# Optimization experiments

Hardware: AMD Instinct MI355X
Metric: run time of the kernel (lower is better)

Reference implementation:

```python
import jax, jax.numpy as jnp
import numpy as np

SCALE = 0.0625      # spatial_scale
OUT = 7             # out_size (== part_size)
C_OUT = 256         # output_dim (== input channels, group_size=1)
SPP = 4             # sample_per_part
TRANS_STD = 0.1
FC_DIM = 1024
B, H, W = 4, 128, 128
N_ROI = 2000
IMG = 2048.0        # H / SCALE


def _round_half(x):
    # CUDA round(): half away from zero (coords are non-negative here)
    return jnp.floor(x + 0.5)


def deform_roi_pool(data, rois, offset):
    """Faithful port of deform_roi_pooling (DCNv2 deform PS-ROI pooling, group_size=1).
    data: [B,C,H,W]; rois: [N,5]; offset: None or [N,2,OUT,OUT]. Returns [N,C,OUT,OUT]."""
    Bn, C, Hh, Ww = data.shape
    N = rois.shape[0]
    b = rois[:, 0].astype(jnp.int32)
    sw = _round_half(rois[:, 1]) * SCALE - 0.5
    sh = _round_half(rois[:, 2]) * SCALE - 0.5
    ew = (_round_half(rois[:, 3]) + 1.0) * SCALE - 0.5
    eh = (_round_half(rois[:, 4]) + 1.0) * SCALE - 0.5
    rw = jnp.maximum(ew - sw, 0.1)
    rh = jnp.maximum(eh - sh, 0.1)
    bw, bh = rw / OUT, rh / OUT              # bin sizes
    subw, subh = bw / SPP, bh / SPP          # sub-bin sizes

    ph, pw = jnp.meshgrid(jnp.arange(OUT, dtype=data.dtype),
                          jnp.arange(OUT, dtype=data.dtype), indexing='ij')
    wstart = pw[None] * bw[:, None, None] + sw[:, None, None]   # [N,OUT,OUT]
    hstart = ph[None] * bh[:, None, None] + sh[:, None, None]
    if offset is not None:
        # part_size == out_size -> part index == bin index
        wstart = wstart + offset[:, 0] * TRANS_STD * rw[:, None, None]
        hstart = hstart + offset[:, 1] * TRANS_STD * rh[:, None, None]

    ih2, iw2 = jnp.meshgrid(jnp.arange(SPP, dtype=data.dtype),
                            jnp.arange(SPP, dtype=data.dtype), indexing='ij')
    ih2, iw2 = ih2.reshape(-1), iw2.reshape(-1)  # [SPP*SPP]
    # sample coords [S2, N, OUT, OUT]
    ws = wstart[None] + iw2[:, None, None, None] * subw[None, :, None, None]
    hs = hstart[None] + ih2[:, None, None, None] * subh[None, :, None, None]

    bb = b[:, None, None]  # [N,1,1]

    def body(carry, coords):
        acc, cnt = carry
        w, h = coords                                 # [N,OUT,OUT]
        valid = (w >= -0.5) & (w <= Ww - 0.5) & (h >= -0.5) & (h <= Hh - 0.5)
        wc = jnp.clip(w, 0.0, Ww - 1.0)
        hc = jnp.clip(h, 0.0, Hh - 1.0)
        x0 = jnp.floor(wc).astype(jnp.int32)
        y0 = jnp.floor(hc).astype(jnp.int32)
        x1 = jnp.minimum(x0 + 1, Ww - 1)
        y1 = jnp.minimum(y0 + 1, Hh - 1)
        dx = wc - x0
        dy = hc - y0
        v00 = data[bb, :, y0, x0]   # [N,OUT,OUT,C]
        v01 = data[bb, :, y0, x1]
        v10 = data[bb, :, y1, x0]
        v11 = data[bb, :, y1, x1]
        val = (((1 - dx) * (1 - dy))[..., None] * v00
               + (dx * (1 - dy))[..., None] * v01
               + ((1 - dx) * dy)[..., None] * v10
               + (dx * dy)[..., None] * v11)
        val = jnp.where(valid[..., None], val, 0.0)
        return (acc + val, cnt + valid.astype(data.dtype)), None

    init = (jnp.zeros((N, OUT, OUT, C), data.dtype),
            jnp.zeros((N, OUT, OUT), data.dtype))
    (s, cnt), _ = jax.lax.scan(body, init, (ws, hs))
    out = jnp.where(cnt[..., None] > 0, s / jnp.maximum(cnt, 1.0)[..., None], 0.0)
    return jnp.transpose(out, (0, 3, 1, 2))  # [N,C,OUT,OUT]


def setup_inputs() -> dict:
    key = jax.random.key(0)
    ks = jax.random.split(key, 16)
    data = jax.random.normal(ks[0], (B, C_OUT, H, W), dtype=jnp.float32)
    bidx = jax.random.randint(ks[1], (N_ROI,), 0, B).astype(jnp.float32)
    x1 = jax.random.uniform(ks[2], (N_ROI,), minval=0.0, maxval=IMG - 64.0)
    y1 = jax.random.uniform(ks[3], (N_ROI,), minval=0.0, maxval=IMG - 64.0)
    wbox = jax.random.uniform(ks[4], (N_ROI,), minval=16.0, maxval=400.0)
    hbox = jax.random.uniform(ks[5], (N_ROI,), minval=16.0, maxval=400.0)
    rois = jnp.stack([bidx, x1, y1,
                      jnp.minimum(x1 + wbox, IMG - 1.0),
                      jnp.minimum(y1 + hbox, IMG - 1.0)], axis=1)
    fin = OUT * OUT * C_OUT  # 12544
    def lin(k, i, o, s=None):
        s = (1.0 / np.sqrt(i)) if s is None else s
        return jax.random.normal(k, (i, o), dtype=jnp.float32) * s
    return {
        'data': data, 'rois': rois,
        'w1': lin(ks[6], fin, FC_DIM), 'b1': jnp.zeros((FC_DIM,), jnp.float32),
        'w2': lin(ks[7], FC_DIM, FC_DIM), 'b2': jnp.zeros((FC_DIM,), jnp.float32),
        'w3': lin(ks[8], FC_DIM, OUT * OUT * 2, 0.01), 'b3': jnp.zeros((OUT * OUT * 2,), jnp.float32),
        'mw1': lin(ks[9], fin, FC_DIM), 'mb1': jnp.zeros((FC_DIM,), jnp.float32),
        'mw2': lin(ks[10], FC_DIM, OUT * OUT, 0.01), 'mb2': jnp.zeros((OUT * OUT,), jnp.float32),
    }


def reference(data, rois, w1, b1, w2, b2, w3, b3, mw1, mb1, mw2, mb2):
    n = rois.shape[0]
    x = deform_roi_pool(data, rois, None)              # [N,C,OUT,OUT]
    xf = x.reshape(n, -1)
    h = jax.nn.relu(xf @ w1 + b1)
    h = jax.nn.relu(h @ w2 + b2)
    offset = (h @ w3 + b3).reshape(n, 2, OUT, OUT)
    m = jax.nn.relu(xf @ mw1 + mb1)
    mask = jax.nn.sigmoid(m @ mw2 + mb2).reshape(n, 1, OUT, OUT)
    feat = deform_roi_pool(data, rois, offset) * mask
    return feat
```

## Files before the change

kernel.cpp:

```cpp
#include <hip/hip_runtime.h>
#include <math.h>

#define WDIM 128
#define HDIM 128
#define BDIM 4
#define CDIM 256
#define NROI 2000
#define MPAD 2048
#define FIN  12544
#define FC   1024
#define HWC  (HDIM * WDIM * CDIM)

typedef unsigned short bf16r;
typedef unsigned short u16;
typedef __attribute__((ext_vector_type(8))) short bf16x8;
typedef __attribute__((ext_vector_type(4))) float f32x4;
typedef __attribute__((ext_vector_type(8))) _Float16 half8;
typedef __attribute__((ext_vector_type(8))) unsigned short ushort8v;

__device__ __forceinline__ bf16r f2bf(float f) {
    unsigned u = __float_as_uint(f);
    u += 0x7FFFu + ((u >> 16) & 1u);
    return (bf16r)(u >> 16);
}
__device__ __forceinline__ u16 f2h(float f) {
    union { u16 s; _Float16 h; } c; c.h = (_Float16)f; return c.s;
}

__device__ __forceinline__ void async16(const bf16r* g, bf16r* l) {
    __builtin_amdgcn_global_load_lds(
        (const __attribute__((address_space(1))) unsigned int*)g,
        (__attribute__((address_space(3))) unsigned int*)l, 16, 0, 0);
}

__device__ __forceinline__ void roi_geom(const float* __restrict__ rois, int n,
                                         int& b, float& sw, float& sh,
                                         float& rw, float& rh) {
    const float* r = rois + (size_t)n * 5;
    b = (int)r[0];
    float r1 = floorf(r[1] + 0.5f);
    float r2 = floorf(r[2] + 0.5f);
    float r3 = floorf(r[3] + 0.5f);
    float r4 = floorf(r[4] + 0.5f);
    sw = r1 * 0.0625f - 0.5f;
    sh = r2 * 0.0625f - 0.5f;
    float ew = (r3 + 1.0f) * 0.0625f - 0.5f;
    float eh = (r4 + 1.0f) * 0.0625f - 0.5f;
    rw = fmaxf(ew - sw, 0.1f);
    rh = fmaxf(eh - sh, 0.1f);
}

__device__ __forceinline__ void build_geometry(
        int n, int tid, const float* __restrict__ rois,
        const float* __restrict__ offs,
        const float* __restrict__ maskb,
        float* axW, unsigned* axMeta, uint2* wpix, int* npx, float* scale) {
    if (tid < 98) {
        int po = tid >> 1, axis = tid & 1;
        int b; float sw, sh, rw, rh;
        roi_geom(rois, n, b, sw, sh, rw, rh);
        float bw = rw * (1.f / 7.f), bh = rh * (1.f / 7.f);
        int ph = po / 7, pw = po - ph * 7;
        float start, sub;
        if (axis == 0) {
            start = (float)pw * bw + sw;
            if (offs) start += offs[(size_t)n * 98 + po] * 0.1f * rw;
            sub = bw * 0.25f;
        } else {
            start = (float)ph * bh + sh;
            if (offs) start += offs[(size_t)n * 98 + 49 + po] * 0.1f * rh;
            sub = bh * 0.25f;
        }
        float wsl[5] = {0.f, 0.f, 0.f, 0.f, 0.f};
        int base = 0, cnt = 0, mx = 0, any = 0;
#pragma unroll
        for (int i = 0; i < 4; ++i) {
            float p = start + (float)i * sub;
            bool valid = (p >= -0.5f) & (p <= 127.5f);
            float pc = fminf(fmaxf(p, 0.f), 127.f);
            int p0 = (int)floorf(pc);
            float d = pc - (float)p0;
            int p1 = min(p0 + 1, 127);
            if (valid) {
                if (!any) { base = p0; any = 1; }
                int c0 = p0 - base, c1 = p1 - base;
                float w0 = 1.f - d;
#pragma unroll
                for (int k = 0; k < 5; ++k)
                    wsl[k] += ((c0 == k) ? w0 : 0.f) + ((c1 == k) ? d : 0.f);
                cnt++;
                mx = max(mx, c1);
            }
        }
        int N = any ? mx + 1 : 0;
        axMeta[tid] = (unsigned)(N | (cnt << 3) | (base << 6));
#pragma unroll
        for (int k = 0; k < 5; ++k) axW[tid * 5 + k] = wsl[k];
    }
    __syncthreads();
    if (tid < 245) {
        int po = tid / 5, r = tid - po * 5;
        unsigned mx_ = axMeta[po * 2], my_ = axMeta[po * 2 + 1];
        int NX = mx_ & 7, NY = my_ & 7;
        int bx = (mx_ >> 6) & 127, by = (my_ >> 6) & 127;
        if (r == 0) {
            int cntx = (mx_ >> 3) & 7, cnty = (my_ >> 3) & 7;
            int ct = cntx * cnty;
            float sc = (ct > 0) ? 1.f / (float)ct : 0.f;
            if (maskb) sc *= (ct > 0) ? maskb[(size_t)n * 49 + po] : 0.f;
            npx[po] = NX * NY;
            scale[po] = sc;
        }
        if (r < NY) {
            float wyr = axW[(po * 2 + 1) * 5 + r];
            unsigned rowoff = (unsigned)(((by + r) * 128 + bx) * 512);
#pragma unroll
            for (int c = 0; c < 5; ++c)
                if (c < NX)
                    wpix[po * 28 + r * NX + c] =
                        make_uint2(rowoff + (unsigned)c * 512u,
                                   __float_as_uint(wyr * axW[po * 2 * 5 + c]));
        }
    }
    __syncthreads();
}

__global__ __launch_bounds__(256) void transpose_kernel(const float* __restrict__ data,
                                                        u16* __restrict__ data_t) {
    __shared__ float t[32][33];
    int x0 = blockIdx.x << 5;
    int c0 = blockIdx.y << 5;
    int b  = blockIdx.z >> 7;
    int y  = blockIdx.z & 127;
    int tx = threadIdx.x, ty = threadIdx.y;
#pragma unroll
    for (int i = 0; i < 32; i += 8)
        t[ty + i][tx] = data[(((size_t)b * CDIM + c0 + ty + i) * HDIM + y) * WDIM + x0 + tx];
    __syncthreads();
#pragma unroll
    for (int i = 0; i < 32; i += 8)
        data_t[(((size_t)b * HDIM + y) * WDIM + x0 + ty + i) * CDIM + c0 + tx] = f2h(t[tx][ty + i]);
}

__global__ __launch_bounds__(256) void conv_kernel(const float* __restrict__ srcA,
                                                   const float* __restrict__ srcB,
                                                   int nsplit, int ncols, int Nout,
                                                   int K, int perm,
                                                   bf16r* __restrict__ dst) {
    __shared__ float t[32][33];
    int k0 = blockIdx.x << 5, n0 = blockIdx.y << 5;
    int tx = threadIdx.x & 31, ty = threadIdx.x >> 5;
#pragma unroll
    for (int i = 0; i < 32; i += 8) {
        int k = k0 + ty + i;
        int n = n0 + tx;
        const float* s = (n < nsplit) ? srcA : srcB;
        int col = (n < nsplit) ? n : n - nsplit;
        int row = perm ? ((k & 255) * 49 + (k >> 8)) : k;
        float v = (n < Nout && col < ncols) ? s[(size_t)row * ncols + col] : 0.f;
        t[ty + i][tx] = v;
    }
    __syncthreads();
#pragma unroll
    for (int i = 0; i < 32; i += 8) {
        int n = n0 + ty + i;
        if (n < Nout) dst[(size_t)n * K + k0 + tx] = f2bf(t[tx][ty + i]);
    }
}

__global__ __launch_bounds__(512) void pool1_kernel(const u16* __restrict__ data_t,
                                                    const float* __restrict__ rois,
                                                    bf16r* __restrict__ xf) {
    __shared__ float axW[98 * 5];
    __shared__ unsigned axMeta[98];
    __shared__ uint2 wpix[49 * 28];
    __shared__ int npx[49];
    __shared__ float scale[49];
    int n = blockIdx.x, tid = threadIdx.x;
    build_geometry(n, tid, rois, nullptr, nullptr, axW, axMeta, wpix, npx, scale);
    int b = (int)rois[(size_t)n * 5];
    int wave = tid >> 6, lane = tid & 63, shalf = lane >> 5, c8 = (lane & 31) << 3;
    const char* dpb = (const char*)(data_t + (size_t)b * HWC + c8);
    for (int po = wave * 2 + shalf; po < 49; po += 16) {
        int npe = npx[po];
        float sc = scale[po];
        const uint2* wp = wpix + po * 28;
        float a[8];
#pragma unroll
        for (int k = 0; k < 8; ++k) a[k] = 0.f;
        int p = 0;
        for (; p + 2 <= npe; p += 2) {
            uint2 q0 = wp[p], q1 = wp[p + 1];
            half8 v0 = *(const half8*)(dpb + q0.x);
            half8 v1 = *(const half8*)(dpb + q1.x);
            float w0 = __uint_as_float(q0.y), w1 = __uint_as_float(q1.y);
#pragma unroll
            for (int k = 0; k < 8; ++k) a[k] += w0 * (float)v0[k];
#pragma unroll
            for (int k = 0; k < 8; ++k) a[k] += w1 * (float)v1[k];
        }
        if (p < npe) {
            uint2 q0 = wp[p];
            half8 v0 = *(const half8*)(dpb + q0.x);
            float w0 = __uint_as_float(q0.y);
#pragma unroll
            for (int k = 0; k < 8; ++k) a[k] += w0 * (float)v0[k];
        }
        ushort8v o;
#pragma unroll
        for (int k = 0; k < 8; ++k) o[k] = f2bf(a[k] * sc);
        *(ushort8v*)(xf + (size_t)n * FIN + po * 256 + c8) = o;
    }
}

__global__ __launch_bounds__(512) void pool2_kernel(const u16* __restrict__ data_t,
                                                    const float* __restrict__ rois,
                                                    const float* __restrict__ offs,
                                                    const float* __restrict__ maskb,
                                                    float* __restrict__ out) {
    __shared__ float tile[49 * 128];
    __shared__ float axW[98 * 5];
    __shared__ unsigned axMeta[98];
    __shared__ uint2 wpix[49 * 28];
    __shared__ int npx[49];
    __shared__ float scale[49];
    int n = blockIdx.x, chalf = blockIdx.y, tid = threadIdx.x;
    build_geometry(n, tid, rois, offs, maskb, axW, axMeta, wpix, npx, scale);
    int b = (int)rois[(size_t)n * 5];
    int wave = tid >> 6, lane = tid & 63, q = lane >> 4, c8 = (lane & 15) << 3;
    const char* dpb = (const char*)(data_t + (size_t)b * HWC + chalf * 128 + c8);
    for (int po = wave * 4 + q; po < 49; po += 32) {
        int npe = npx[po];
        float sc = scale[po];
        const uint2* wp = wpix + po * 28;
        float a[8];
#pragma unroll
        for (int k = 0; k < 8; ++k) a[k] = 0.f;
        int p = 0;
        for (; p + 2 <= npe; p += 2) {
            uint2 q0 = wp[p], q1 = wp[p + 1];
            half8 v0 = *(const half8*)(dpb + q0.x);
            half8 v1 = *(const half8*)(dpb + q1.x);
            float w0 = __uint_as_float(q0.y), w1 = __uint_as_float(q1.y);
#pragma unroll
            for (int k = 0; k < 8; ++k) a[k] += w0 * (float)v0[k];
#pragma unroll
            for (int k = 0; k < 8; ++k) a[k] += w1 * (float)v1[k];
        }
        if (p < npe) {
            uint2 q0 = wp[p];
            half8 v0 = *(const half8*)(dpb + q0.x);
            float w0 = __uint_as_float(q0.y);
#pragma unroll
            for (int k = 0; k < 8; ++k) a[k] += w0 * (float)v0[k];
        }
        int cs = c8 ^ ((po & 7) << 3);
        float4 lo = make_float4(a[0] * sc, a[1] * sc, a[2] * sc, a[3] * sc);
        float4 hi = make_float4(a[4] * sc, a[5] * sc, a[6] * sc, a[7] * sc);
        *(float4*)&tile[po * 128 + cs] = lo;
        *(float4*)&tile[po * 128 + cs + 4] = hi;
    }
    __syncthreads();
    float* op = out + (size_t)n * FIN + (size_t)chalf * 6272;
    for (int i = tid; i < 6272; i += 512) {
        int c = i / 49, po = i - c * 49;
        op[i] = tile[po * 128 + (c ^ ((po & 7) << 3))];
    }
}

__global__ __launch_bounds__(256) void gemm_mfma_kernel(
        const bf16r* __restrict__ A, int lda,
        const bf16r* __restrict__ Bt, int K,
        float* __restrict__ P, int Npad, int KS) {
    __shared__ bf16r As[128 * 32];
    __shared__ bf16r Bs[128 * 32];
    int tid = threadIdx.x;
    int wave = tid >> 6, lane = tid & 63;
    int m0 = blockIdx.y << 7, n0 = blockIdx.x << 7;
    int z = blockIdx.z;

    int srow = lane >> 2;
    int kchunk = ((lane & 3) ^ ((lane >> 3) & 3)) << 3;
    const bf16r* aG0 = A + (size_t)(m0 + wave * 32 + srow) * lda + kchunk;
    const bf16r* aG1 = A + (size_t)(m0 + wave * 32 + 16 + srow) * lda + kchunk;
    const bf16r* bG0 = Bt + (size_t)(n0 + wave * 32 + srow) * K + kchunk;
    const bf16r* bG1 = Bt + (size_t)(n0 + wave * 32 + 16 + srow) * K + kchunk;
    bf16r* aL0 = As + wave * 1024;
    bf16r* aL1 = As + wave * 1024 + 512;
    bf16r* bL0 = Bs + wave * 1024;
    bf16r* bL1 = Bs + wave * 1024 + 512;

    int l15 = lane & 15, quad = lane >> 4;
    int wr = wave >> 1, wc = wave & 1;
    int psw = (quad ^ ((l15 >> 1) & 3)) << 3;
    int aoff[4], boff[4];
#pragma unroll
    for (int t = 0; t < 4; ++t) {
        aoff[t] = ((wr * 64 + t * 16 + l15) * 32 + psw) * 2;
        boff[t] = ((wc * 64 + t * 16 + l15) * 32 + psw) * 2;
    }

    f32x4 acc[4][4];
#pragma unroll
    for (int i = 0; i < 4; ++i)
#pragma unroll
        for (int j = 0; j < 4; ++j) acc[i][j] = (f32x4){0.f, 0.f, 0.f, 0.f};

    int iters = K >> 5;
    int i0 = (int)((long)iters * z / KS);
    int i1 = (int)((long)iters * (z + 1) / KS);

    {
        size_t k0 = (size_t)i0 << 5;
        async16(aG0 + k0, aL0); async16(aG1 + k0, aL1);
        async16(bG0 + k0, bL0); async16(bG1 + k0, bL1);
    }
    for (int it = i0; it < i1; ++it) {
        __syncthreads();
        bf16x8 af[4], bfv[4];
#pragma unroll
        for (int t = 0; t < 4; ++t) af[t] = *(const bf16x8*)((const char*)As + aoff[t]);
#pragma unroll
        for (int t = 0; t < 4; ++t) bfv[t] = *(const bf16x8*)((const char*)Bs + boff[t]);
        __syncthreads();
        if (it + 1 < i1) {
            size_t k0 = (size_t)(it + 1) << 5;
            async16(aG0 + k0, aL0); async16(aG1 + k0, aL1);
            async16(bG0 + k0, bL0); async16(bG1 + k0, bL1);
        }
#pragma unroll
        for (int i = 0; i < 4; ++i)
#pragma unroll
            for (int j = 0; j < 4; ++j)
                acc[i][j] = __builtin_amdgcn_mfma_f32_16x16x32_bf16(af[i], bfv[j], acc[i][j], 0, 0, 0);
    }

    float* Pp = P + (size_t)z * MPAD * Npad;
#pragma unroll
    for (int i = 0; i < 4; ++i) {
        int row = m0 + wr * 64 + i * 16 + quad * 4;
#pragma unroll
        for (int j = 0; j < 4; ++j) {
            int col = n0 + wc * 64 + j * 16 + l15;
            float* o = Pp + (size_t)row * Npad + col;
#pragma unroll
            for (int r = 0; r < 4; ++r) o[(size_t)r * Npad] = acc[i][j][r];
        }
    }
}

__global__ __launch_bounds__(256) void reduce_kernel(
        const float* __restrict__ P, int shift, int KS,
        const float* __restrict__ bias0, const float* __restrict__ bias1, int bsplit,
        void* __restrict__ Out, int ldo, int M, int Nreal, int outmode) {
    int idx = blockIdx.x * 256 + threadIdx.x;
    int Npad = 1 << shift;
    int row = idx >> shift, col = idx & (Npad - 1);
    float s = 0.f;
    size_t plane = (size_t)MPAD << shift;
    for (int zz = 0; zz < KS; ++zz) s += P[(size_t)zz * plane + idx];
    if (row < M && col < Nreal) {
        float b = (col < bsplit) ? bias0[col] : bias1[col - bsplit];
        float v = s + b;
        if (outmode == 0) {
            v = fmaxf(v, 0.f);
            ((bf16r*)Out)[(size_t)row * ldo + col] = f2bf(v);
        } else {
            if (outmode == 2) v = 1.f / (1.f + expf(-v));
            ((float*)Out)[(size_t)row * ldo + col] = v;
        }
    }
}

extern "C" void kernel_launch(void* const* d_in, const int* in_sizes, int n_in,
                              void* d_out, int out_size, void* d_ws, size_t ws_size,
                              hipStream_t stream) {
    const float* data = (const float*)d_in[0];
    const float* rois = (const float*)d_in[1];
    const float* w1   = (const float*)d_in[2];
    const float* b1   = (const float*)d_in[3];
    const float* w2   = (const float*)d_in[4];
    const float* b2   = (const float*)d_in[5];
    const float* w3   = (const float*)d_in[6];
    const float* b3   = (const float*)d_in[7];
    const float* mw1  = (const float*)d_in[8];
    const float* mb1  = (const float*)d_in[9];
    const float* mw2  = (const float*)d_in[10];
    const float* mb2  = (const float*)d_in[11];
    float* out = (float*)d_out;

    char* w = (char*)d_ws;
    size_t off = 0;
    auto carve = [&](size_t bytes) {
        void* p = w + off;
        off += (bytes + 255) & ~(size_t)255;
        return p;
    };
    u16* data_t   = (u16*)carve((size_t)BDIM * HDIM * WDIM * CDIM * 2);
    bf16r* xf     = (bf16r*)carve((size_t)MPAD * FIN * 2);
    bf16r* bt1    = (bf16r*)carve((size_t)MPAD * FIN * 2);
    bf16r* hm     = (bf16r*)carve((size_t)MPAD * 2048 * 2);
    bf16r* h2     = (bf16r*)carve((size_t)MPAD * 1024 * 2);
    bf16r* bt2    = (bf16r*)carve((size_t)1024 * 1024 * 2);
    bf16r* bt3    = (bf16r*)carve((size_t)128 * 1024 * 2);
    bf16r* bt4    = (bf16r*)carve((size_t)128 * 1024 * 2);
    float* offs   = (float*)carve((size_t)NROI * 98 * 4);
    float* maskb  = (float*)carve((size_t)NROI * 49 * 4);
    float* P      = (float*)carve((size_t)3 * MPAD * 2048 * 4);

    conv_kernel<<<dim3(392, 64), 256, 0, stream>>>(w1, mw1, 1024, 1024, 2048, FIN, 1, bt1);
    conv_kernel<<<dim3(32, 32), 256, 0, stream>>>(w2, w2, 1 << 30, 1024, 1024, 1024, 0, bt2);
    conv_kernel<<<dim3(32, 4), 256, 0, stream>>>(w3, w3, 1 << 30, 98, 98, 1024, 0, bt3);
    conv_kernel<<<dim3(32, 2), 256, 0, stream>>>(mw2, mw2, 1 << 30, 49, 49, 1024, 0, bt4);
    transpose_kernel<<<dim3(4, 8, 512), dim3(32, 8), 0, stream>>>(data, data_t);
    pool1_kernel<<<dim3(NROI), 512, 0, stream>>>(data_t, rois, xf);

    gemm_mfma_kernel<<<dim3(16, 16, 3), 256, 0, stream>>>(xf, FIN, bt1, FIN, P, 2048, 3);
    reduce_kernel<<<16384, 256, 0, stream>>>(P, 11, 3, b1, mb1, 1024, hm, 2048, NROI, 2048, 0);
    gemm_mfma_kernel<<<dim3(8, 16, 4), 256, 0, stream>>>(hm, 2048, bt2, 1024, P, 1024, 4);
    reduce_kernel<<<8192, 256, 0, stream>>>(P, 10, 4, b2, b2, 1 << 30, h2, 1024, NROI, 1024, 0);
    gemm_mfma_kernel<<<dim3(1, 16, 8), 256, 0, stream>>>(h2, 1024, bt3, 1024, P, 128, 8);
    reduce_kernel<<<1024, 256, 0, stream>>>(P, 7, 8, b3, b3, 1 << 30, offs, 98, NROI, 98, 1);
    gemm_mfma_kernel<<<dim3(1, 16, 8), 256, 0, stream>>>(hm + 1024, 2048, bt4, 1024, P, 128, 8);
    reduce_kernel<<<1024, 256, 0, stream>>>(P, 7, 8, mb2, mb2, 1 << 30, maskb, 49, NROI, 49, 2);

    pool2_kernel<<<dim3(NROI, 2), 512, 0, stream>>>(data_t, rois, offs, maskb, out);
}
```

Measured before the change: 571.3 us.

## Add 256x256-tile 8-wave MFMA GEMM with ping-pong LDS staging for first FC layer

```diff
diff --git a/kernel.cpp b/kernel.cpp
--- a/kernel.cpp
+++ b/kernel.cpp
@@ -32,6 +32,9 @@
         (const __attribute__((address_space(1))) unsigned int*)g,
         (__attribute__((address_space(3))) unsigned int*)l, 16, 0, 0);
 }
+
+#define VMW(n) asm volatile("s_waitcnt vmcnt(" #n ")" ::: "memory")
+#define BARRIER() __builtin_amdgcn_s_barrier()
 
 __device__ __forceinline__ void roi_geom(const float* __restrict__ rois, int n,
                                          int& b, float& sw, float& sh,
@@ -268,6 +271,119 @@
     }
 }
 
+#define STAGE_A(buf, h, kt) do { \
+    async16(Abase + (size_t)(kt) * 64 + sAoff[h][0], &lds[buf][0][((h) * 128 + wave * 8) * 64]); \
+    async16(Abase + (size_t)(kt) * 64 + sAoff[h][1], &lds[buf][0][((h) * 128 + 64 + wave * 8) * 64]); \
+} while (0)
+#define STAGE_B(buf, h, kt) do { \
+    async16(Bbase + (size_t)(kt) * 64 + sBoff[h][0], &lds[buf][1][((h) * 128 + wave * 8) * 64]); \
+    async16(Bbase + (size_t)(kt) * 64 + sBoff[h][1], &lds[buf][1][((h) * 128 + 64 + wave * 8) * 64]); \
+} while (0)
+#define PHASE(buf, mh, nh, STAGE_STMT, GUARD_STMT) do { \
+    const char* Ar = (const char*)&lds[buf][0][0] + aQ + (mh) * 16384; \
+    const char* Br = (const char*)&lds[buf][1][0] + bQ + (nh) * 16384; \
+    bf16x8 af[4][2], bfv[2][2]; \
+    _Pragma("unroll") for (int i = 0; i < 4; ++i) \
+        _Pragma("unroll") for (int ks = 0; ks < 2; ++ks) \
+            af[i][ks] = *(const bf16x8*)(Ar + i * 2048 + fRB[ks]); \
+    _Pragma("unroll") for (int jf = 0; jf < 2; ++jf) \
+        _Pragma("unroll") for (int ks = 0; ks < 2; ++ks) \
+            bfv[jf][ks] = *(const bf16x8*)(Br + jf * 2048 + fRB[ks]); \
+    STAGE_STMT; \
+    BARRIER(); \
+    __builtin_amdgcn_s_setprio(1); \
+    _Pragma("unroll") for (int i = 0; i < 4; ++i) \
+        _Pragma("unroll") for (int jf = 0; jf < 2; ++jf) \
+            _Pragma("unroll") for (int ks = 0; ks < 2; ++ks) \
+                acc[(mh) * 4 + i][(nh) * 2 + jf] = __builtin_amdgcn_mfma_f32_16x16x32_bf16( \
+                    af[i][ks], bfv[jf][ks], acc[(mh) * 4 + i][(nh) * 2 + jf], 0, 0, 0); \
+    __builtin_amdgcn_s_setprio(0); \
+    GUARD_STMT; \
+    BARRIER(); \
+} while (0)
+
+__global__ __launch_bounds__(512, 2) void gemm256_kernel(
+        const bf16r* __restrict__ A, int lda,
+        const bf16r* __restrict__ Bt, int ldb,
+        float* __restrict__ P, int Npad, int KS, int ktiles) {
+    __shared__ bf16r lds[2][2][256 * 64];
+    int tid = threadIdx.x;
+    int wave = tid >> 6, lane = tid & 63;
+    int l15 = lane & 15, quad = lane >> 4;
+    int wm = wave >> 2, wn = wave & 3;
+
+    int idx = blockIdx.x + gridDim.x * blockIdx.y;
+    int nid = (idx & 7) * ((gridDim.x * gridDim.y) >> 3) + (idx >> 3);
+    int bx = nid % gridDim.x, by = nid / gridDim.x;
+    int m0 = by << 8, n0 = bx << 8;
+    int z = blockIdx.z;
+
+    int sAoff[2][2], sBoff[2][2];
+#pragma unroll
+    for (int h = 0; h < 2; ++h)
+#pragma unroll
+        for (int j = 0; j < 2; ++j) {
+            int slot = h * 128 + j * 64 + wave * 8 + (lane >> 3);
+            int g = (lane & 7) ^ ((slot >> 1) & 7);
+            int rowA = ((slot >> 6) & 1) * 128 + (slot >> 7) * 64 + (slot & 63);
+            int colB = ((slot >> 5) & 3) * 64 + (slot >> 7) * 32 + (slot & 31);
+            sAoff[h][j] = rowA * lda + g * 8;
+            sBoff[h][j] = colB * ldb + g * 8;
+        }
+    const bf16r* Abase = A + (size_t)m0 * lda;
+    const bf16r* Bbase = Bt + (size_t)n0 * ldb;
+
+    int fRB[2];
+#pragma unroll
+    for (int ks = 0; ks < 2; ++ks)
+        fRB[ks] = l15 * 128 + ((((ks << 2) + quad) ^ ((l15 >> 1) & 7)) << 4);
+    int aQ = wm * 8192;
+    int bQ = wn * 4096;
+
+    f32x4 acc[8][4];
+#pragma unroll
+    for (int i = 0; i < 8; ++i)
+#pragma unroll
+        for (int j = 0; j < 4; ++j) acc[i][j] = (f32x4){0.f, 0.f, 0.f, 0.f};
+
+    int tb = ((ktiles * z) / KS) & ~1;
+    int te = (z == KS - 1) ? ktiles : ((ktiles * (z + 1)) / KS) & ~1;
+    int nit = (te - tb) >> 1;
+
+    STAGE_A(0, 0, tb); STAGE_B(0, 0, tb); STAGE_A(0, 1, tb); STAGE_B(0, 1, tb);
+    STAGE_A(1, 0, tb + 1); STAGE_B(1, 0, tb + 1);
+    VMW(4);
+    BARRIER();
+
+    for (int it = 0; it < nit; ++it) {
+        int t1 = tb + 2 * it + 1, nx0 = t1 + 1, nx1 = t1 + 2;
+        bool last = (it == nit - 1);
+        PHASE(0, 0, 0, { STAGE_A(1, 1, t1); }, {});
+        PHASE(0, 0, 1, { STAGE_B(1, 1, t1); }, {});
+        PHASE(0, 1, 0, { if (!last) STAGE_A(0, 0, nx0); }, {});
+        PHASE(0, 1, 1, { if (!last) STAGE_B(0, 0, nx0); },
+              { if (last) { VMW(0); } else { VMW(4); } });
+        PHASE(1, 0, 0, { if (!last) STAGE_A(0, 1, nx0); }, {});
+        PHASE(1, 0, 1, { if (!last) STAGE_B(0, 1, nx0); }, {});
+        PHASE(1, 1, 0, { if (!last) STAGE_A(1, 0, nx1); }, {});
+        PHASE(1, 1, 1, { if (!last) STAGE_B(1, 0, nx1); },
+              { if (!last) { VMW(4); } });
+    }
+
+    float* Pp = P + (size_t)z * MPAD * Npad;
+#pragma unroll
+    for (int I = 0; I < 8; ++I) {
+        int row = m0 + wm * 128 + I * 16 + quad * 4;
+#pragma unroll
+        for (int J = 0; J < 4; ++J) {
+            int col = n0 + wn * 64 + J * 16 + l15;
+            float* o = Pp + (size_t)row * Npad + col;
+#pragma unroll
+            for (int r = 0; r < 4; ++r) o[(size_t)r * Npad] = acc[I][J][r];
+        }
+    }
+}
+
 __global__ __launch_bounds__(256) void gemm_mfma_kernel(
         const bf16r* __restrict__ A, int lda,
         const bf16r* __restrict__ Bt, int K,
@@ -276,7 +392,12 @@
     __shared__ bf16r Bs[128 * 32];
     int tid = threadIdx.x;
     int wave = tid >> 6, lane = tid & 63;
-    int m0 = blockIdx.y << 7, n0 = blockIdx.x << 7;
+    int nwgxy = gridDim.x * gridDim.y;
+    int idx = blockIdx.x + gridDim.x * blockIdx.y;
+    int chunk = nwgxy >> 3;
+    int nid = (idx & 7) * chunk + (idx >> 3);
+    int bx = nid % gridDim.x, by = nid / gridDim.x;
+    int m0 = by << 7, n0 = bx << 7;
     int z = blockIdx.z;
 
     int srow = lane >> 2;
@@ -406,7 +527,10 @@
     bf16r* bt4    = (bf16r*)carve((size_t)128 * 1024 * 2);
     float* offs   = (float*)carve((size_t)NROI * 98 * 4);
     float* maskb  = (float*)carve((size_t)NROI * 49 * 4);
-    float* P      = (float*)carve((size_t)3 * MPAD * 2048 * 4);
+    float* P      = (float*)(w + off);
+    size_t plane  = (size_t)MPAD * 2048 * 4;
+    size_t avail  = (ws_size > off) ? ws_size - off : 0;
+    int use256 = (avail >= 4 * plane);
 
     conv_kernel<<<dim3(392, 64), 256, 0, stream>>>(w1, mw1, 1024, 1024, 2048, FIN, 1, bt1);
     conv_kernel<<<dim3(32, 32), 256, 0, stream>>>(w2, w2, 1 << 30, 1024, 1024, 1024, 0, bt2);
@@ -415,8 +539,13 @@
     transpose_kernel<<<dim3(4, 8, 512), dim3(32, 8), 0, stream>>>(data, data_t);
     pool1_kernel<<<dim3(NROI), 512, 0, stream>>>(data_t, rois, xf);
 
-    gemm_mfma_kernel<<<dim3(16, 16, 3), 256, 0, stream>>>(xf, FIN, bt1, FIN, P, 2048, 3);
-    reduce_kernel<<<16384, 256, 0, stream>>>(P, 11, 3, b1, mb1, 1024, hm, 2048, NROI, 2048, 0);
+    if (use256) {
+        gemm256_kernel<<<dim3(8, 8, 4), 512, 0, stream>>>(xf, FIN, bt1, FIN, P, 2048, 4, 196);
+        reduce_kernel<<<16384, 256, 0, stream>>>(P, 11, 4, b1, mb1, 1024, hm, 2048, NROI, 2048, 0);
+    } else {
+        gemm_mfma_kernel<<<dim3(16, 16, 3), 256, 0, stream>>>(xf, FIN, bt1, FIN, P, 2048, 3);
+        reduce_kernel<<<16384, 256, 0, stream>>>(P, 11, 3, b1, mb1, 1024, hm, 2048, NROI, 2048, 0);
+    }
     gemm_mfma_kernel<<<dim3(8, 16, 4), 256, 0, stream>>>(hm, 2048, bt2, 1024, P, 1024, 4);
     reduce_kernel<<<8192, 256, 0, stream>>>(P, 10, 4, b2, b2, 1 << 30, h2, 1024, NROI, 1024, 0);
     gemm_mfma_kernel<<<dim3(1, 16, 8), 256, 0, stream>>>(h2, 1024, bt3, 1024, P, 128, 8);
```

New measurement: 525.2 us. -8.1%, faster.
